# Kernel tuning notes

Measured on AMD Instinct MI355X. Metric: run time of the kernel, lower is better.

## Reference

```python
import jax, jax.numpy as jnp
import numpy as np

T, B, DZ, DH, DS = 1000, 256, 64, 256, 16


def setup_inputs() -> dict:
    key = jax.random.key(0)
    k = jax.random.split(key, 6)
    r_w1 = 1.0 / np.sqrt(DZ)   # init_uniform_same: r = 1/sqrt(last dim)
    r_w2 = 1.0 / np.sqrt(DH)
    r_c = 1.0 / np.sqrt(DS)
    # W_trial=True: same initial matrix repeated across trials
    W1 = jnp.tile(jax.random.uniform(k[0], (DH, DZ), minval=-r_w1, maxval=r_w1), (B, 1, 1))
    W2 = jnp.tile(jax.random.uniform(k[1], (DZ, DH), minval=-r_w2, maxval=r_w2), (B, 1, 1))
    C = jax.random.uniform(k[2], (DZ, DS), minval=-r_c, maxval=r_c)
    A = jnp.full((DZ,), 0.95, dtype=jnp.float32)
    h1 = jax.random.normal(k[3], (DH,), dtype=jnp.float32)
    h2 = jax.random.normal(k[4], (DZ,), dtype=jnp.float32)
    kz, ks = jax.random.split(k[5])
    z0 = jax.random.normal(kz, (B, DZ), dtype=jnp.float32)
    s = jax.random.normal(ks, (T, B, DS), dtype=jnp.float32) * 0.1
    return {"z0": z0, "s": s, "A": A, "W1": W1, "W2": W2, "h1": h1, "h2": h2, "C": C}


def reference(z0, s, A, W1, W2, h1, h2, C):
    # Precompute external-input projection for all steps: s_t @ C.T  -> [T, B, DZ]
    Cs = jnp.einsum('tbs,zs->tbz', s, C)

    def step(z, cs_t):
        # per-trial W1: Wz = einsum('ij,ijk->ik', z, W1^T) == einsum('bj,bhj->bh', z, W1)
        Wz = jnp.einsum('bj,bhj->bh', z, W1)                       # [B, DH]
        z_act = jax.nn.relu(Wz + h1) - jax.nn.relu(Wz)             # clipped shPLRNN nonlinearity
        z_new = A * z + jnp.einsum('bh,bzh->bz', z_act, W2) + h2 + cs_t
        return z_new, z_new

    _, z_seq = jax.lax.scan(step, z0, Cs)  # z_seq: [T, B, DZ]
    return z_seq
```

## Files before the change

kernel.cpp:

```cpp
#include <hip/hip_runtime.h>

#define T_STEPS 1000
#define NB 256
#define DZ 64
#define DH 256
#define DS 16
#define CHUNK 64
#define NCHUNK 16

__device__ __forceinline__ void barrier_lgkm() {
    asm volatile("s_waitcnt lgkmcnt(0)\n\ts_barrier" ::: "memory");
}

template<int CTRL>
__device__ __forceinline__ float dpp_add(float x) {
    int y = __builtin_amdgcn_update_dpp(0, __float_as_int(x), CTRL, 0xF, 0xF, true);
    return x + __int_as_float(y);
}
__device__ __forceinline__ float row16_allsum(float x) {
    x = dpp_add<0x128>(x);
    x = dpp_add<0x124>(x);
    x = dpp_add<0x122>(x);
    x = dpp_add<0x121>(x);
    return x;
}

__global__ __launch_bounds__(1024)
__attribute__((amdgpu_waves_per_eu(4, 4)))
void plrnn_scan(const float* __restrict__ z0, const float* __restrict__ s,
                const float* __restrict__ A,  const float* __restrict__ W1,
                const float* __restrict__ W2, const float* __restrict__ h1,
                const float* __restrict__ h2, const float* __restrict__ C,
                float* __restrict__ out)
{
    const int tid = threadIdx.x;
    const int b   = blockIdx.x;
    const int h   = tid >> 2;
    const int q   = tid & 3;
    const int j   = tid >> 4;
    const int r4  = tid & 15;

    __shared__ __align__(16) float z_sh[DZ];
    __shared__ __align__(16) float za_sh[320];
    __shared__ __align__(16) float s_sh[CHUNK * DS];

    float4 w1v[4];
    {
        const float4* p = (const float4*)(W1 + (size_t)b * DH * DZ) + 4 * tid;
        #pragma unroll
        for (int k = 0; k < 4; ++k) w1v[k] = p[k];
    }
    float4 w2v[4];
    {
        const float4* p = (const float4*)(W2 + (size_t)b * DZ * DH) + 4 * tid;
        #pragma unroll
        for (int k = 0; k < 4; ++k) w2v[k] = p[k];
    }
    const float cj  = C[tid];

    const float h1r = h1[h];
    const float rsgn = (h1r > 0.f) ?  1.f : -1.f;
    const float roff = (h1r > 0.f) ?  h1r :  0.f;
    const float rlo  = fminf(h1r, 0.f);
    const float rhi  = fmaxf(h1r, 0.f);

    const float Aj   = A[j];
    const float h2j16 = h2[j] * 0.0625f;
    float zr = z0[b * DZ + j];

    if (tid < DZ) z_sh[tid] = z0[b * DZ + tid];

    const int srow = tid >> 4, scol = tid & 15;
    float sreg = s[(size_t)min(srow, T_STEPS - 1) * NB * DS + (size_t)b * DS + scol];

    const int zi = h + ((h >> 4) << 2);
    const int bj = b * DZ + j;

    const float4* const z4   = (const float4*)(z_sh + 16 * q);
    const float4* const q4   = (const float4*)(za_sh + 20 * r4);
    const float* const  sp_l = s_sh + r4;

    __syncthreads();

    for (int ci = 0; ci < NCHUNK; ++ci) {
        const int t0 = ci * CHUNK;
        s_sh[tid] = sreg;
        {
            int tl = min(t0 + CHUNK + srow, T_STEPS - 1);
            sreg = s[(size_t)tl * NB * DS + (size_t)b * DS + scol];
        }

        #pragma unroll 4
        for (int tt = 0; tt < CHUNK; ++tt) {
            float a0 = 0.f, a1 = 0.f, a2 = 0.f, a3 = 0.f;
            #pragma unroll
            for (int k = 0; k < 4; ++k) {
                float4 zv = z4[k];
                a0 = fmaf(w1v[k].x, zv.x, a0);
                a1 = fmaf(w1v[k].y, zv.y, a1);
                a2 = fmaf(w1v[k].z, zv.z, a2);
                a3 = fmaf(w1v[k].w, zv.w, a3);
            }
            float p1 = (a0 + a1) + (a2 + a3);
            p1 = dpp_add<0xB1>(p1);
            p1 = dpp_add<0x4E>(p1);
            float za = __builtin_amdgcn_fmed3f(fmaf(rsgn, p1, roff), rlo, rhi);
            if (q == 0) za_sh[zi] = za;
            barrier_lgkm();

            float sv = sp_l[tt * DS];
            float p00 = fmaf(cj, sv, h2j16);
            float p01 = 0.f, p02 = 0.f, p03 = 0.f;
            #pragma unroll
            for (int k = 0; k < 4; ++k) {
                float4 v = q4[k];
                p00 = fmaf(w2v[k].x, v.x, p00);
                p01 = fmaf(w2v[k].y, v.y, p01);
                p02 = fmaf(w2v[k].z, v.z, p02);
                p03 = fmaf(w2v[k].w, v.w, p03);
            }
            float pa = (p00 + p01) + (p02 + p03);
            pa = row16_allsum(pa);

            float zn = fmaf(Aj, zr, pa);
            zr = zn;
            if (r4 == 0) z_sh[j] = zn;
            barrier_lgkm();

            const int t = t0 + tt;
            if (r4 == 0 && t < T_STEPS)
                out[(size_t)t * (NB * DZ) + bj] = zn;
        }
    }
}

extern "C" void kernel_launch(void* const* d_in, const int* in_sizes, int n_in,
                              void* d_out, int out_size, void* d_ws, size_t ws_size,
                              hipStream_t stream) {
    const float* z0p = (const float*)d_in[0];
    const float* sp  = (const float*)d_in[1];
    const float* Ap  = (const float*)d_in[2];
    const float* W1p = (const float*)d_in[3];
    const float* W2p = (const float*)d_in[4];
    const float* h1p = (const float*)d_in[5];
    const float* h2p = (const float*)d_in[6];
    const float* Cp  = (const float*)d_in[7];

    plrnn_scan<<<dim3(NB), dim3(1024), 0, stream>>>(z0p, sp, Ap, W1p, W2p, h1p, h2p, Cp,
                                                    (float*)d_out);
}
```

Baseline: 606.5 us.

## Use wave-local readlane broadcast and LDS atomic accumulation for one barrier per step

Each wave now owns 16 hidden units and broadcasts its clipped activations within the wave via readlane, instead of going through shared memory. Every wave then forms partial sums for all 64 outputs and adds them into a triple-buffered LDS accumulator with workgroup-scope atomics. This cuts the per-step barriers from two to one. The cost is LDS atomic contention from 16 waves on 64 addresses, scalar readlane traffic, and output writes that lag one step behind.

```diff
diff --git a/kernel.cpp b/kernel.cpp
--- a/kernel.cpp
+++ b/kernel.cpp
@@ -17,12 +17,8 @@
     int y = __builtin_amdgcn_update_dpp(0, __float_as_int(x), CTRL, 0xF, 0xF, true);
     return x + __int_as_float(y);
 }
-__device__ __forceinline__ float row16_allsum(float x) {
-    x = dpp_add<0x128>(x);
-    x = dpp_add<0x124>(x);
-    x = dpp_add<0x122>(x);
-    x = dpp_add<0x121>(x);
-    return x;
+__device__ __forceinline__ float rdlane(float v, int lane) {
+    return __int_as_float(__builtin_amdgcn_readlane(__float_as_int(v), lane));
 }
 
 __global__ __launch_bounds__(1024)
@@ -35,102 +31,115 @@
 {
     const int tid = threadIdx.x;
     const int b   = blockIdx.x;
-    const int h   = tid >> 2;
-    const int q   = tid & 3;
-    const int j   = tid >> 4;
-    const int r4  = tid & 15;
+    const int w   = tid >> 6;
+    const int l   = tid & 63;
+    const int q   = l & 3;
+    const int k   = l >> 2;
+    const int h   = (w << 4) | k;
 
-    __shared__ __align__(16) float z_sh[DZ];
-    __shared__ __align__(16) float za_sh[320];
-    __shared__ __align__(16) float s_sh[CHUNK * DS];
+    __shared__ __align__(16) float zbuf[3][DZ];
 
     float4 w1v[4];
     {
-        const float4* p = (const float4*)(W1 + (size_t)b * DH * DZ) + 4 * tid;
+        const float4* p = (const float4*)(W1 + (size_t)b * DH * DZ + (size_t)h * DZ + 16 * q);
         #pragma unroll
-        for (int k = 0; k < 4; ++k) w1v[k] = p[k];
+        for (int i = 0; i < 4; ++i) w1v[i] = p[i];
     }
     float4 w2v[4];
     {
-        const float4* p = (const float4*)(W2 + (size_t)b * DZ * DH) + 4 * tid;
+        const float4* p = (const float4*)(W2 + (size_t)b * DZ * DH + (size_t)l * DH + 16 * w);
         #pragma unroll
-        for (int k = 0; k < 4; ++k) w2v[k] = p[k];
+        for (int i = 0; i < 4; ++i) w2v[i] = p[i];
     }
-    const float cj  = C[tid];
+    const float cw = C[(l << 4) | w];
 
-    const float h1r = h1[h];
+    const float h1r  = h1[h];
     const float rsgn = (h1r > 0.f) ?  1.f : -1.f;
     const float roff = (h1r > 0.f) ?  h1r :  0.f;
     const float rlo  = fminf(h1r, 0.f);
     const float rhi  = fmaxf(h1r, 0.f);
 
-    const float Aj   = A[j];
-    const float h2j16 = h2[j] * 0.0625f;
-    float zr = z0[b * DZ + j];
+    const float Aj  = A[l];
+    const float h2j = h2[l];
 
-    if (tid < DZ) z_sh[tid] = z0[b * DZ + tid];
+    if (tid < DZ) {
+        zbuf[0][tid] = z0[b * DZ + tid];
+        zbuf[1][tid] = 0.f;
+        zbuf[2][tid] = 0.f;
+    }
 
-    const int srow = tid >> 4, scol = tid & 15;
-    float sreg = s[(size_t)min(srow, T_STEPS - 1) * NB * DS + (size_t)b * DS + scol];
+    const size_t sbase = (size_t)b * DS + w;
+    float sregA = s[(size_t)min(l, T_STEPS - 1) * (NB * DS) + sbase];
+    float sregB;
 
-    const int zi = h + ((h >> 4) << 2);
-    const int bj = b * DZ + j;
-
-    const float4* const z4   = (const float4*)(z_sh + 16 * q);
-    const float4* const q4   = (const float4*)(za_sh + 20 * r4);
-    const float* const  sp_l = s_sh + r4;
+    float* bc = &zbuf[0][0];
+    float* bn = &zbuf[1][0];
+    float* bo = &zbuf[2][0];
 
     __syncthreads();
 
     for (int ci = 0; ci < NCHUNK; ++ci) {
         const int t0 = ci * CHUNK;
-        s_sh[tid] = sreg;
         {
-            int tl = min(t0 + CHUNK + srow, T_STEPS - 1);
-            sreg = s[(size_t)tl * NB * DS + (size_t)b * DS + scol];
+            int tl = min(t0 + CHUNK + l, T_STEPS - 1);
+            sregB = s[(size_t)tl * (NB * DS) + sbase];
         }
 
         #pragma unroll 4
         for (int tt = 0; tt < CHUNK; ++tt) {
+            const int g = t0 + tt;
+
+            const float4* z4 = (const float4*)bc + 4 * q;
+            float4 zv0 = z4[0], zv1 = z4[1], zv2 = z4[2], zv3 = z4[3];
             float a0 = 0.f, a1 = 0.f, a2 = 0.f, a3 = 0.f;
-            #pragma unroll
-            for (int k = 0; k < 4; ++k) {
-                float4 zv = z4[k];
-                a0 = fmaf(w1v[k].x, zv.x, a0);
-                a1 = fmaf(w1v[k].y, zv.y, a1);
-                a2 = fmaf(w1v[k].z, zv.z, a2);
-                a3 = fmaf(w1v[k].w, zv.w, a3);
-            }
+            a0 = fmaf(w1v[0].x, zv0.x, a0); a1 = fmaf(w1v[0].y, zv0.y, a1);
+            a2 = fmaf(w1v[0].z, zv0.z, a2); a3 = fmaf(w1v[0].w, zv0.w, a3);
+            a0 = fmaf(w1v[1].x, zv1.x, a0); a1 = fmaf(w1v[1].y, zv1.y, a1);
+            a2 = fmaf(w1v[1].z, zv1.z, a2); a3 = fmaf(w1v[1].w, zv1.w, a3);
+            a0 = fmaf(w1v[2].x, zv2.x, a0); a1 = fmaf(w1v[2].y, zv2.y, a1);
+            a2 = fmaf(w1v[2].z, zv2.z, a2); a3 = fmaf(w1v[2].w, zv2.w, a3);
+            a0 = fmaf(w1v[3].x, zv3.x, a0); a1 = fmaf(w1v[3].y, zv3.y, a1);
+            a2 = fmaf(w1v[3].z, zv3.z, a2); a3 = fmaf(w1v[3].w, zv3.w, a3);
             float p1 = (a0 + a1) + (a2 + a3);
             p1 = dpp_add<0xB1>(p1);
             p1 = dpp_add<0x4E>(p1);
             float za = __builtin_amdgcn_fmed3f(fmaf(rsgn, p1, roff), rlo, rhi);
-            if (q == 0) za_sh[zi] = za;
+
+            float sv = rdlane(sregA, tt);
+            float p00 = fmaf(cw, sv, 0.f), p01 = 0.f, p02 = 0.f, p03 = 0.f;
+            p00 = fmaf(w2v[0].x, rdlane(za,  0), p00);
+            p01 = fmaf(w2v[0].y, rdlane(za,  4), p01);
+            p02 = fmaf(w2v[0].z, rdlane(za,  8), p02);
+            p03 = fmaf(w2v[0].w, rdlane(za, 12), p03);
+            p00 = fmaf(w2v[1].x, rdlane(za, 16), p00);
+            p01 = fmaf(w2v[1].y, rdlane(za, 20), p01);
+            p02 = fmaf(w2v[1].z, rdlane(za, 24), p02);
+            p03 = fmaf(w2v[1].w, rdlane(za, 28), p03);
+            p00 = fmaf(w2v[2].x, rdlane(za, 32), p00);
+            p01 = fmaf(w2v[2].y, rdlane(za, 36), p01);
+            p02 = fmaf(w2v[2].z, rdlane(za, 40), p02);
+            p03 = fmaf(w2v[2].w, rdlane(za, 44), p03);
+            p00 = fmaf(w2v[3].x, rdlane(za, 48), p00);
+            p01 = fmaf(w2v[3].y, rdlane(za, 52), p01);
+            p02 = fmaf(w2v[3].z, rdlane(za, 56), p02);
+            p03 = fmaf(w2v[3].w, rdlane(za, 60), p03);
+
+            float zj = 0.f;
+            if (w == 1) {
+                zj = bc[l];
+                p00 = fmaf(Aj, zj, p00) + h2j;
+            }
+            float acc = (p00 + p01) + (p02 + p03);
+            __hip_atomic_fetch_add(&bn[l], acc, __ATOMIC_RELAXED,
+                                   __HIP_MEMORY_SCOPE_WORKGROUP);
+            if (w == 2) bo[l] = 0.f;
+            if (w == 1 && g >= 1 && g <= T_STEPS)
+                out[(size_t)(g - 1) * (NB * DZ) + b * DZ + l] = zj;
+
+            float* tmp = bc; bc = bn; bn = bo; bo = tmp;
             barrier_lgkm();
-
-            float sv = sp_l[tt * DS];
-            float p00 = fmaf(cj, sv, h2j16);
-            float p01 = 0.f, p02 = 0.f, p03 = 0.f;
-            #pragma unroll
-            for (int k = 0; k < 4; ++k) {
-                float4 v = q4[k];
-                p00 = fmaf(w2v[k].x, v.x, p00);
-                p01 = fmaf(w2v[k].y, v.y, p01);
-                p02 = fmaf(w2v[k].z, v.z, p02);
-                p03 = fmaf(w2v[k].w, v.w, p03);
-            }
-            float pa = (p00 + p01) + (p02 + p03);
-            pa = row16_allsum(pa);
-
-            float zn = fmaf(Aj, zr, pa);
-            zr = zn;
-            if (r4 == 0) z_sh[j] = zn;
-            barrier_lgkm();
-
-            const int t = t0 + tt;
-            if (r4 == 0 && t < T_STEPS)
-                out[(size_t)t * (NB * DZ) + bj] = zn;
         }
+        sregA = sregB;
     }
 }
 
```

After: 1.696 ms. 2.8x slower.
